# Kernel tuning notes

Measured on AMD Instinct MI355X. Metric: run time of the kernel, lower is better.

Reference implementation:

```python
import jax, jax.numpy as jnp
import numpy as np

ALPHA = 0.2  # LeakyReLU negative slope
NEG_BIG = -9e15


def setup_inputs() -> dict:
    key = jax.random.key(0)
    k1, k2, k3, k4 = jax.random.split(key, 4)
    N, F_IN, F_OUT = 8192, 256, 128
    h = jax.random.normal(k1, (N, F_IN), dtype=jnp.float32)
    adj = jax.random.randint(k2, (N, N), 0, 2, dtype=jnp.int32)
    # xavier_uniform with gain=1.414
    def xavier(k, shape, gain=1.414):
        fan_in, fan_out = shape[0], shape[1]
        bound = gain * np.sqrt(6.0 / (fan_in + fan_out))
        return jax.random.uniform(k, shape, jnp.float32, -bound, bound)
    W = xavier(k3, (F_IN, F_OUT))
    a = xavier(k4, (2 * F_OUT, 1))
    return {"h": h, "adj": adj, "W": W, "a": a}


def reference(h, adj, W, a):
    # Wh: [N, F_out]
    Wh = h @ W
    F_out = W.shape[1]
    a1 = a[:F_out, 0]   # attends to source (row) node
    a2 = a[F_out:, 0]   # attends to target (col) node
    # Additive decomposition of concat([Wh_i, Wh_j]) @ a:
    # e[i, j] = leaky_relu(Wh_i . a1 + Wh_j . a2)
    f1 = Wh @ a1  # [N]
    f2 = Wh @ a2  # [N]
    e = jax.nn.leaky_relu(f1[:, None] + f2[None, :], negative_slope=ALPHA)  # [N, N]
    scores = jnp.where(adj > 0, e, jnp.float32(NEG_BIG))
    attention = jax.nn.softmax(scores, axis=1)
    # dropout is identity in eval mode (training=False)
    h_prime = attention @ Wh  # [N, F_out]
    return h_prime
```

## Files before the change

kernel.cpp:

```cpp
#include <hip/hip_runtime.h>


#define N_NODES 8192
#define F_IN 256
#define F_OUT 128
#define RPB 32
#define JCH 128
#define JSPLIT 2
#define JRANGE (N_NODES / JSPLIT)
#define NCH (JRANGE / JCH)

typedef _Float16 half8 __attribute__((ext_vector_type(8)));
typedef float floatx4 __attribute__((ext_vector_type(4)));
typedef float f32x4 __attribute__((ext_vector_type(4)));

__device__ __align__(16) float g_Wh[N_NODES * F_OUT];
__device__ __align__(16) _Float16 g_WhT[(size_t)F_OUT * N_NODES];
__device__ __align__(16) float g_f1[N_NODES];
__device__ __align__(16) float g_f2[N_NODES];
__device__ __align__(16) float g_part[JSPLIT][N_NODES * F_OUT];
__device__ __align__(16) float g_spart[JSPLIT][N_NODES];

#define GLD16(lds, gp)                                                        \
  __builtin_amdgcn_global_load_lds(                                           \
      (const __attribute__((address_space(1))) unsigned int*)(gp),            \
      (__attribute__((address_space(3))) unsigned int*)(lds), 16, 0, 0)

__global__ __launch_bounds__(256, 2) void wh_kernel(
    const float* __restrict__ h, const float* __restrict__ W) {
  __shared__ float hT[F_IN][20];
  const int t = threadIdx.x;
  const int i0 = blockIdx.x * 16;
  {
    const int row = t >> 4;
    const int fu = t & 15;
#pragma unroll
    for (int r = 0; r < 4; ++r) {
      const int ku = r * 16 + fu;
      const float4 v = *(const float4*)(h + (size_t)(i0 + row) * F_IN + ku * 4);
      hT[ku * 4 + 0][row] = v.x; hT[ku * 4 + 1][row] = v.y;
      hT[ku * 4 + 2][row] = v.z; hT[ku * 4 + 3][row] = v.w;
    }
  }
  __syncthreads();
  const int c = t & 127;
  const int rg = t >> 7;
  float acc[8];
#pragma unroll
  for (int r = 0; r < 8; ++r) acc[r] = 0.f;
#pragma unroll 8
  for (int k = 0; k < F_IN; ++k) {
    const float wv = W[k * F_OUT + c];
    const float4 x0 = *(const float4*)(&hT[k][rg * 8]);
    const float4 x1 = *(const float4*)(&hT[k][rg * 8 + 4]);
    acc[0] = fmaf(x0.x, wv, acc[0]); acc[1] = fmaf(x0.y, wv, acc[1]);
    acc[2] = fmaf(x0.z, wv, acc[2]); acc[3] = fmaf(x0.w, wv, acc[3]);
    acc[4] = fmaf(x1.x, wv, acc[4]); acc[5] = fmaf(x1.y, wv, acc[5]);
    acc[6] = fmaf(x1.z, wv, acc[6]); acc[7] = fmaf(x1.w, wv, acc[7]);
  }
#pragma unroll
  for (int r = 0; r < 8; ++r)
    g_Wh[(size_t)(i0 + rg * 8 + r) * F_OUT + c] = acc[r];
  union { _Float16 hh[8]; uint4 u4; } pk;
#pragma unroll
  for (int r = 0; r < 8; ++r) pk.hh[r] = (_Float16)acc[r];
  *(uint4*)(g_WhT + (size_t)c * N_NODES + i0 + rg * 8) = pk.u4;
}

__global__ __launch_bounds__(256) void f12_kernel(const float* __restrict__ a) {
  const int t = threadIdx.x;
  const int row = blockIdx.x * 2 + (t >> 7);
  const int c = t & 127;
  const float wh = g_Wh[(size_t)row * F_OUT + c];
  float p1 = wh * a[c];
  float p2 = wh * a[F_OUT + c];
  for (int o = 32; o > 0; o >>= 1) {
    p1 += __shfl_down(p1, o, 64);
    p2 += __shfl_down(p2, o, 64);
  }
  __shared__ float s1[4], s2[4];
  const int w = t >> 6;
  if ((t & 63) == 0) { s1[w] = p1; s2[w] = p2; }
  __syncthreads();
  if ((t & 127) == 0) {
    g_f1[row] = s1[w] + s1[w + 1];
    g_f2[row] = s2[w] + s2[w + 1];
  }
}

__device__ __forceinline__ float score_p(int a, float f2v, float f1r) {
  float s = f1r + f2v;
  s = fmaxf(s, 0.2f * s);
  float arg = (a > 0) ? fmaf(s, 1.44269504088896f, -16.0f) : -1.0e5f;
  return __builtin_amdgcn_exp2f(arg);
}

__global__ __launch_bounds__(256, 2) void gat_attn_kernel(const int* __restrict__ adj) {
  const int t = threadIdx.x;
  const int wave = t >> 6;
  const int lane = t & 63;
  const int mrow = lane & 15;
  const int quad = lane >> 4;
  const int i0 = blockIdx.x * RPB;
  const int js = blockIdx.y;
  const int jbase = js * JRANGE;

  __shared__ int ldsAdj[2][RPB * JCH];
  __shared__ float ldsF2[2][256];
  __shared__ float ldsO[RPB][F_OUT];
  __shared__ float ldsS[4][RPB];

  int rm[4], cm[4];
  {
    half8 a1f, b1f, a2f, b2f;
#pragma unroll
    for (int e = 0; e < 8; ++e) {
      a1f[e] = (_Float16)0; b1f[e] = (_Float16)0;
      a2f[e] = (_Float16)0; b2f[e] = (_Float16)0;
    }
    if (quad == 0) {
      a1f[0] = (_Float16)mrow; b1f[0] = (_Float16)1;
      a2f[0] = (_Float16)1;    b2f[0] = (_Float16)mrow;
    }
    floatx4 d1 = (floatx4)0.f, d2 = (floatx4)0.f;
    d1 = __builtin_amdgcn_mfma_f32_16x16x32_f16(a1f, b1f, d1, 0, 0, 0);
    d2 = __builtin_amdgcn_mfma_f32_16x16x32_f16(a2f, b2f, d2, 0, 0, 0);
#pragma unroll
    for (int r = 0; r < 4; ++r) { rm[r] = (int)d1[r]; cm[r] = (int)d2[r]; }
  }

  const float f1r0 = g_f1[i0 + mrow];
  const float f1r1 = g_f1[i0 + 16 + mrow];

  half8 ones;
#pragma unroll
  for (int e = 0; e < 8; ++e) ones[e] = (_Float16)1;

  floatx4 acc[2][8];
  floatx4 asum[2];
#pragma unroll
  for (int tl = 0; tl < 2; ++tl) {
    asum[tl] = (floatx4)0.f;
#pragma unroll
    for (int ct = 0; ct < 8; ++ct) acc[tl][ct] = (floatx4)0.f;
  }

#define DMA(cc, bb) do {                                                      \
    _Pragma("unroll")                                                         \
    for (int R = 0; R < 4; ++R) {                                             \
      const int m = R * 8 + wave * 2 + (lane >> 5);                           \
      const int u = ((lane & 31) - m) & 31;                                   \
      const int* gp = adj + (size_t)(i0 + m) * N_NODES + jbase + (cc) * JCH + u * 4; \
      GLD16(&ldsAdj[bb][(R * 8 + wave * 2) * JCH], gp);                       \
    }                                                                         \
    if (wave == 0) {                                                          \
      int idx = jbase + (cc) * JCH + lane * 4;                                \
      idx = idx > (N_NODES - 4) ? (N_NODES - 4) : idx;                        \
      GLD16(&ldsF2[bb][0], g_f2 + idx);                                       \
    }                                                                         \
  } while (0)

  DMA(0, 0);
  __builtin_amdgcn_s_waitcnt(0);
  __syncthreads();

#pragma unroll 1
  for (int c = 0; c < NCH; ++c) {
    const int b = c & 1;
    const int jloc = wave * 32 + quad * 8;
    const int jglob = jbase + c * JCH + jloc;

    half8 bfr[8];
#pragma unroll
    for (int ct = 0; ct < 8; ++ct)
      bfr[ct] = *(const half8*)(g_WhT + (size_t)(ct * 16 + mrow) * N_NODES + jglob);

    if (c + 1 < NCH) DMA(c + 1, b ^ 1);

    const int u0 = jloc >> 2;
    const char* base = (const char*)&ldsAdj[b][0];
    const int4 A00 = *(const int4*)(base + mrow * 512 + (((u0 + mrow) & 31) << 4));
    const int4 A01 = *(const int4*)(base + mrow * 512 + (((u0 + 1 + mrow) & 31) << 4));
    const int m2 = mrow + 16;
    const int4 A10 = *(const int4*)(base + m2 * 512 + (((u0 + m2) & 31) << 4));
    const int4 A11 = *(const int4*)(base + m2 * 512 + (((u0 + 1 + m2) & 31) << 4));
    const float4 F0 = *(const float4*)&ldsF2[b][jloc];
    const float4 F1 = *(const float4*)&ldsF2[b][jloc + 4];

    half8 af0, af1;
    af0[0] = (_Float16)score_p(A00.x, F0.x, f1r0);
    af0[1] = (_Float16)score_p(A00.y, F0.y, f1r0);
    af0[2] = (_Float16)score_p(A00.z, F0.z, f1r0);
    af0[3] = (_Float16)score_p(A00.w, F0.w, f1r0);
    af0[4] = (_Float16)score_p(A01.x, F1.x, f1r0);
    af0[5] = (_Float16)score_p(A01.y, F1.y, f1r0);
    af0[6] = (_Float16)score_p(A01.z, F1.z, f1r0);
    af0[7] = (_Float16)score_p(A01.w, F1.w, f1r0);
    af1[0] = (_Float16)score_p(A10.x, F0.x, f1r1);
    af1[1] = (_Float16)score_p(A10.y, F0.y, f1r1);
    af1[2] = (_Float16)score_p(A10.z, F0.z, f1r1);
    af1[3] = (_Float16)score_p(A10.w, F0.w, f1r1);
    af1[4] = (_Float16)score_p(A11.x, F1.x, f1r1);
    af1[5] = (_Float16)score_p(A11.y, F1.y, f1r1);
    af1[6] = (_Float16)score_p(A11.z, F1.z, f1r1);
    af1[7] = (_Float16)score_p(A11.w, F1.w, f1r1);

#pragma unroll
    for (int ct = 0; ct < 8; ++ct) {
      acc[0][ct] = __builtin_amdgcn_mfma_f32_16x16x32_f16(af0, bfr[ct], acc[0][ct], 0, 0, 0);
      acc[1][ct] = __builtin_amdgcn_mfma_f32_16x16x32_f16(af1, bfr[ct], acc[1][ct], 0, 0, 0);
    }
    asum[0] = __builtin_amdgcn_mfma_f32_16x16x32_f16(af0, ones, asum[0], 0, 0, 0);
    asum[1] = __builtin_amdgcn_mfma_f32_16x16x32_f16(af1, ones, asum[1], 0, 0, 0);

    __builtin_amdgcn_s_waitcnt(0);
    __syncthreads();
  }
#undef DMA

  if (mrow == 0) {
#pragma unroll
    for (int tl = 0; tl < 2; ++tl)
#pragma unroll
      for (int r = 0; r < 4; ++r)
        ldsS[wave][tl * 16 + rm[r]] = asum[tl][r];
  }
  for (int w = 0; w < 4; ++w) {
    if (wave == w) {
#pragma unroll
      for (int tl = 0; tl < 2; ++tl)
#pragma unroll
        for (int ct = 0; ct < 8; ++ct)
#pragma unroll
          for (int r = 0; r < 4; ++r) {
            float* p = &ldsO[tl * 16 + rm[r]][ct * 16 + cm[r]];
            if (w == 0) *p = acc[tl][ct][r];
            else        *p += acc[tl][ct][r];
          }
    }
    __syncthreads();
  }
  {
    const int row = t >> 3;
    const int c0 = (t & 7) * 16;
    float* dst = g_part[js] + (size_t)(i0 + row) * F_OUT + c0;
#pragma unroll
    for (int q = 0; q < 4; ++q)
      *(f32x4*)(dst + q * 4) = *(const f32x4*)(&ldsO[row][c0 + q * 4]);
    if (t < RPB)
      g_spart[js][i0 + t] = ldsS[0][t] + ldsS[1][t] + ldsS[2][t] + ldsS[3][t];
  }
}

__global__ __launch_bounds__(256) void comb_kernel(float* __restrict__ out) {
  const int u = blockIdx.x * 256 + threadIdx.x;
  const int row = u >> 5;
  const float s = g_spart[0][row] + g_spart[1][row];
  const f32x4 v = ((const f32x4*)g_part[0])[u] + ((const f32x4*)g_part[1])[u];
  ((f32x4*)out)[u] = v * (1.0f / s);
}

extern "C" void kernel_launch(void* const* d_in, const int* in_sizes, int n_in,
                              void* d_out, int out_size, void* d_ws, size_t ws_size,
                              hipStream_t stream) {
  const float* h = (const float*)d_in[0];
  const int* adj = (const int*)d_in[1];
  const float* W = (const float*)d_in[2];
  const float* a = (const float*)d_in[3];
  float* out = (float*)d_out;
  (void)d_ws; (void)ws_size;

  wh_kernel<<<dim3(N_NODES / 16), dim3(256), 0, stream>>>(h, W);
  f12_kernel<<<dim3(N_NODES / 2), dim3(256), 0, stream>>>(a);
  gat_attn_kernel<<<dim3(N_NODES / RPB, JSPLIT), dim3(256), 0, stream>>>(adj);
  comb_kernel<<<dim3(N_NODES * F_OUT / 4 / 256), dim3(256), 0, stream>>>(out);
}
```

Measured before the change: 421.1 us.

## Load adjacency directly into registers and preload f2 slice once, drop per-chunk barriers

Replaces the double-buffered global-to-LDS DMA of adjacency tiles with direct per-thread int4 global loads into registers, and loads the block's entire f2 range into LDS once up front. This removes the per-iteration waitcnt and __syncthreads and the LDS round trip for adj. The cost is that adj loads are no longer prefetched one chunk ahead, so their latency has to be hidden by occupancy and instruction scheduling, and each lane now reads scattered 32-byte pieces from 16 different rows.

```diff
diff --git a/kernel.cpp b/kernel.cpp
--- a/kernel.cpp
+++ b/kernel.cpp
@@ -20,11 +20,6 @@
 __device__ __align__(16) float g_f2[N_NODES];
 __device__ __align__(16) float g_part[JSPLIT][N_NODES * F_OUT];
 __device__ __align__(16) float g_spart[JSPLIT][N_NODES];
-
-#define GLD16(lds, gp)                                                        \
-  __builtin_amdgcn_global_load_lds(                                           \
-      (const __attribute__((address_space(1))) unsigned int*)(gp),            \
-      (__attribute__((address_space(3))) unsigned int*)(lds), 16, 0, 0)
 
 __global__ __launch_bounds__(256, 2) void wh_kernel(
     const float* __restrict__ h, const float* __restrict__ W) {
@@ -105,8 +100,7 @@
   const int js = blockIdx.y;
   const int jbase = js * JRANGE;
 
-  __shared__ int ldsAdj[2][RPB * JCH];
-  __shared__ float ldsF2[2][256];
+  __shared__ float ldsF2[JRANGE];
   __shared__ float ldsO[RPB][F_OUT];
   __shared__ float ldsS[4][RPB];
 
@@ -145,47 +139,33 @@
     for (int ct = 0; ct < 8; ++ct) acc[tl][ct] = (floatx4)0.f;
   }
 
-#define DMA(cc, bb) do {                                                      \
-    _Pragma("unroll")                                                         \
-    for (int R = 0; R < 4; ++R) {                                             \
-      const int m = R * 8 + wave * 2 + (lane >> 5);                           \
-      const int u = ((lane & 31) - m) & 31;                                   \
-      const int* gp = adj + (size_t)(i0 + m) * N_NODES + jbase + (cc) * JCH + u * 4; \
-      GLD16(&ldsAdj[bb][(R * 8 + wave * 2) * JCH], gp);                       \
-    }                                                                         \
-    if (wave == 0) {                                                          \
-      int idx = jbase + (cc) * JCH + lane * 4;                                \
-      idx = idx > (N_NODES - 4) ? (N_NODES - 4) : idx;                        \
-      GLD16(&ldsF2[bb][0], g_f2 + idx);                                       \
-    }                                                                         \
-  } while (0)
-
-  DMA(0, 0);
-  __builtin_amdgcn_s_waitcnt(0);
+#pragma unroll
+  for (int it = 0; it < 4; ++it) {
+    const int u = it * 256 + t;
+    *(float4*)&ldsF2[u * 4] = *(const float4*)(g_f2 + jbase + u * 4);
+  }
   __syncthreads();
+
+  const size_t rowoff0 = (size_t)(i0 + mrow) * N_NODES;
+  const size_t rowoff1 = (size_t)(i0 + 16 + mrow) * N_NODES;
+  const int jloc = wave * 32 + quad * 8;
 
 #pragma unroll 1
   for (int c = 0; c < NCH; ++c) {
-    const int b = c & 1;
-    const int jloc = wave * 32 + quad * 8;
     const int jglob = jbase + c * JCH + jloc;
+
+    const int4 A00 = *(const int4*)(adj + rowoff0 + jglob);
+    const int4 A01 = *(const int4*)(adj + rowoff0 + jglob + 4);
+    const int4 A10 = *(const int4*)(adj + rowoff1 + jglob);
+    const int4 A11 = *(const int4*)(adj + rowoff1 + jglob + 4);
 
     half8 bfr[8];
 #pragma unroll
     for (int ct = 0; ct < 8; ++ct)
       bfr[ct] = *(const half8*)(g_WhT + (size_t)(ct * 16 + mrow) * N_NODES + jglob);
 
-    if (c + 1 < NCH) DMA(c + 1, b ^ 1);
-
-    const int u0 = jloc >> 2;
-    const char* base = (const char*)&ldsAdj[b][0];
-    const int4 A00 = *(const int4*)(base + mrow * 512 + (((u0 + mrow) & 31) << 4));
-    const int4 A01 = *(const int4*)(base + mrow * 512 + (((u0 + 1 + mrow) & 31) << 4));
-    const int m2 = mrow + 16;
-    const int4 A10 = *(const int4*)(base + m2 * 512 + (((u0 + m2) & 31) << 4));
-    const int4 A11 = *(const int4*)(base + m2 * 512 + (((u0 + 1 + m2) & 31) << 4));
-    const float4 F0 = *(const float4*)&ldsF2[b][jloc];
-    const float4 F1 = *(const float4*)&ldsF2[b][jloc + 4];
+    const float4 F0 = *(const float4*)&ldsF2[c * JCH + jloc];
+    const float4 F1 = *(const float4*)&ldsF2[c * JCH + jloc + 4];
 
     half8 af0, af1;
     af0[0] = (_Float16)score_p(A00.x, F0.x, f1r0);
@@ -212,11 +192,7 @@
     }
     asum[0] = __builtin_amdgcn_mfma_f32_16x16x32_f16(af0, ones, asum[0], 0, 0, 0);
     asum[1] = __builtin_amdgcn_mfma_f32_16x16x32_f16(af1, ones, asum[1], 0, 0, 0);
-
-    __builtin_amdgcn_s_waitcnt(0);
-    __syncthreads();
-  }
-#undef DMA
+  }
 
   if (mrow == 0) {
 #pragma unroll
```

New measurement: 451.7 us. 1.07x slower.
